# Optimization experiments

Hardware: AMD Instinct MI355X
Metric: run time of the kernel (lower is better)

The kernel has to match this reference:

```python
import jax, jax.numpy as jnp
import numpy as np

HEADS = 4
DIM_HEAD = 32
SCALE = DIM_HEAD ** -0.5

# Energy conventions (Hopfield / Lagrangian formulation):
#  Neuron(x): g = activation(x); e = sum(x*g) - L(x)
#  Synapse(g, x): e = -sum(g*x)
#  identity Lagrangian: L(x) = 0.5*sum(x^2), g = x  => Conv2d block energy = -0.5*sum(x^2)
#  softmax Lagrangian: L(x) = sum(logsumexp(x, -1)), g = softmax(x, -1)

def setup_inputs() -> dict:
    key = jax.random.key(0)
    ks = jax.random.split(key, 5)
    b, c, h, w = 8, 256, 48, 48
    hidden = HEADS * DIM_HEAD  # 128
    return {
        "x": jax.random.normal(ks[0], (b, c, h, w), jnp.float32),
        "w_qkv": jax.random.normal(ks[1], (hidden * 3, c), jnp.float32) * 0.02,
        "b_qkv": jax.random.normal(ks[2], (hidden * 3,), jnp.float32) * 0.02,
        "w_out": jax.random.normal(ks[3], (c, hidden), jnp.float32) * 0.02,
        "b_out": jax.random.normal(ks[4], (c,), jnp.float32) * 0.02,
    }

def reference(x, w_qkv, b_qkv, w_out, b_out):
    b, c, h, w = x.shape
    # 1x1 conv == channel matmul
    qkv = jnp.einsum('oc,bcxy->boxy', w_qkv, x) + b_qkv[None, :, None, None]
    e_qkv = -0.5 * jnp.sum(qkv * qkv)  # identity-Lagrangian neuron + synapse energy
    q, k, v = jnp.split(qkv, 3, axis=1)
    # 'b (h c) x y -> b h c (x y)'
    def heads(t):
        return t.reshape(b, HEADS, DIM_HEAD, h * w)
    q, k, v = heads(q), heads(k), heads(v)
    q = q * SCALE
    sim = jnp.einsum('bhdi,bhdj->bhij', q, k)  # [b, heads, hw, hw]
    sim = sim - jax.lax.stop_gradient(jnp.max(sim, axis=-1, keepdims=True))
    attn = jax.nn.softmax(sim, axis=-1)
    # softmax-Lagrangian neuron energy: sum(sim*attn) - sum(logsumexp(sim, -1))
    e_attn = jnp.sum(sim * attn) - jnp.sum(jax.nn.logsumexp(sim, axis=-1))
    out = jnp.einsum('bhij,bhdj->bhid', attn, v)  # [b, heads, hw, dim_head]
    # 'b h (x y) d -> b (h d) x y'
    out = out.transpose(0, 1, 3, 2).reshape(b, HEADS * DIM_HEAD, h, w)
    out = jnp.einsum('oc,bcxy->boxy', w_out, out) + b_out[None, :, None, None]
    e_out = -0.5 * jnp.sum(out * out)
    return out, e_attn + e_out + e_qkv
```

## Files before the change

kernel.cpp:

```cpp
#include <hip/hip_runtime.h>
#include <hip/hip_bf16.h>

#define HW 2304
#define NB 8
#define NC 256
#define HID 128
#define DH 32
#define NH 4
#define SCALE 0.17677669529663687f
#define LOG2E 1.4426950408889634f
#define LN2   0.6931471805599453f

using bf16x8 = __attribute__((ext_vector_type(8))) short;
using f32x4  = __attribute__((ext_vector_type(4))) float;

__device__ __forceinline__ short f2bf(float f) {
    unsigned u = __float_as_uint(f);
    u += 0x7FFF + ((u >> 16) & 1);
    return (short)(u >> 16);
}
__device__ __forceinline__ unsigned pk2bf(float a, float b) {
    union { __hip_bfloat162 h; unsigned u; } cv;
    cv.h = __float22bfloat162_rn(float2{a, b});
    return cv.u;
}
__device__ __forceinline__ void gld16(const void* g, void* l) {
    __builtin_amdgcn_global_load_lds(
        (const __attribute__((address_space(1))) unsigned*)g,
        (__attribute__((address_space(3))) unsigned*)l, 16, 0, 0);
}

__global__ __launch_bounds__(256)
void prep(const float* __restrict__ x, const float* __restrict__ wq,
          const float* __restrict__ wo, short* __restrict__ Xt,
          short* __restrict__ Wq, short* __restrict__ Wo, float* __restrict__ wsz)
{
    if (blockIdx.z == 8) {
        const int bid = blockIdx.x + 72 * blockIdx.y;
        if (bid == 0 && threadIdx.x == 0) { wsz[0] = 0.f; ((int*)wsz)[1] = 0; }
        const int i = bid * 256 + threadIdx.x;
        if (i < 384 * 256) Wq[i] = f2bf(wq[i]);
        if (i < 256 * 128) Wo[i] = f2bf(wo[i]);
        return;
    }
    __shared__ float T[32][33];
    const int b = blockIdx.z, c0 = blockIdx.y * 32, s0 = blockIdx.x * 32;
    const int ts = threadIdx.x & 31, tc = threadIdx.x >> 5;
    #pragma unroll
    for (int cc = tc; cc < 32; cc += 8)
        T[cc][ts] = x[((size_t)b * NC + c0 + cc) * HW + s0 + ts];
    __syncthreads();
    const int tcc = threadIdx.x & 31, tss = threadIdx.x >> 5;
    #pragma unroll
    for (int ss = tss; ss < 32; ss += 8)
        Xt[((size_t)b * HW + s0 + ss) * NC + c0 + tcc] = f2bf(T[tcc][ss]);
}

template<int KD, bool QKV>
__global__ __launch_bounds__(256, 4)
void conv_mfma(const short* __restrict__ A, const short* __restrict__ Bt,
               const float* __restrict__ bias, float* __restrict__ out0,
               short* __restrict__ Qb, short* __restrict__ Kb,
               short* __restrict__ Vb, float* __restrict__ E,
               int* __restrict__ ticket, int nblocks, float* __restrict__ edst)
{
    const int b  = blockIdx.z;
    const int bm = blockIdx.y * 64;
    const int bn = blockIdx.x * 128;
    const int t  = threadIdx.x;
    const int w  = t >> 6, lane = t & 63;
    const int n16 = lane & 15, quad = lane >> 4;

    __shared__ __align__(16) char csm[24576];
    __shared__ float red[4];

    const int rL = lane >> 2, cswz = (lane & 3) ^ (rL & 3);
    const char* agl = (const char*)(A  + (size_t)(bm + rL) * KD + cswz * 8);
    const char* bgl = (const char*)(Bt + ((size_t)b * HW + bn + rL) * KD + cswz * 8);

    auto issue = [&](int kc, int pbuf) {
        char* base = csm + pbuf * 12288;
        if (w == 0) {
            gld16(agl + (size_t)(0 * 16 * KD + kc) * 2, base + 0 * 1024);
            gld16(agl + (size_t)(1 * 16 * KD + kc) * 2, base + 1 * 1024);
            gld16(bgl + (size_t)(0 * 16 * KD + kc) * 2, base + 4096 + 0 * 1024);
        } else if (w == 1) {
            gld16(agl + (size_t)(2 * 16 * KD + kc) * 2, base + 2 * 1024);
            gld16(agl + (size_t)(3 * 16 * KD + kc) * 2, base + 3 * 1024);
            gld16(bgl + (size_t)(1 * 16 * KD + kc) * 2, base + 4096 + 1 * 1024);
        } else if (w == 2) {
            gld16(bgl + (size_t)(2 * 16 * KD + kc) * 2, base + 4096 + 2 * 1024);
            gld16(bgl + (size_t)(3 * 16 * KD + kc) * 2, base + 4096 + 3 * 1024);
            gld16(bgl + (size_t)(4 * 16 * KD + kc) * 2, base + 4096 + 4 * 1024);
        } else {
            gld16(bgl + (size_t)(5 * 16 * KD + kc) * 2, base + 4096 + 5 * 1024);
            gld16(bgl + (size_t)(6 * 16 * KD + kc) * 2, base + 4096 + 6 * 1024);
            gld16(bgl + (size_t)(7 * 16 * KD + kc) * 2, base + 4096 + 7 * 1024);
        }
    };

    f32x4 acc[4][2] = {};
    const int rsw = (quad ^ (n16 & 3)) * 16;
    constexpr int NI = KD / 32;

    issue(0, 0);
    for (int ki = 0; ki < NI; ++ki) {
        const int p = ki & 1;
        __syncthreads();
        if (ki + 1 < NI) issue((ki + 1) * 32, p ^ 1);

        const char* Ap = csm + p * 12288;
        const char* Bp = Ap + 4096;
        bf16x8 am[4], bq[2];
        #pragma unroll
        for (int tm = 0; tm < 4; ++tm)
            am[tm] = *(const bf16x8*)(Ap + tm * 1024 + n16 * 64 + rsw);
        #pragma unroll
        for (int j = 0; j < 2; ++j)
            bq[j] = *(const bf16x8*)(Bp + (w * 2 + j) * 1024 + n16 * 64 + rsw);
        #pragma unroll
        for (int tm = 0; tm < 4; ++tm)
            #pragma unroll
            for (int j = 0; j < 2; ++j)
                acc[tm][j] = __builtin_amdgcn_mfma_f32_16x16x32_bf16(am[tm], bq[j], acc[tm][j], 0, 0, 0);
    }

    float e = 0.f;
    #pragma unroll
    for (int tm = 0; tm < 4; ++tm) {
        const int o0 = bm + tm * 16 + quad * 4;
        const float4 bb = *(const float4*)(bias + o0);
        #pragma unroll
        for (int j = 0; j < 2; ++j) {
            const int s = bn + (w * 2 + j) * 16 + n16;
            float v[4] = {acc[tm][j][0] + bb.x, acc[tm][j][1] + bb.y,
                          acc[tm][j][2] + bb.z, acc[tm][j][3] + bb.w};
            e -= 0.5f * (v[0]*v[0] + v[1]*v[1] + v[2]*v[2] + v[3]*v[3]);
            if (QKV) {
                if (o0 < HID) {
                    const int h = o0 >> 5, dh0 = o0 & 31;
                    const float qs = SCALE * LOG2E;
                    short4 pk = {f2bf(v[0]*qs), f2bf(v[1]*qs),
                                 f2bf(v[2]*qs), f2bf(v[3]*qs)};
                    *(short4*)(Qb + ((size_t)(b * NH + h) * HW + s) * DH + dh0) = pk;
                } else if (o0 < 2 * HID) {
                    const int c = o0 - HID, h = c >> 5, dh0 = c & 31;
                    const int g = s & 31;
                    const int sp = (s & ~31) | ((g & 1) << 4) | (g >> 1);
                    short4 pk = {f2bf(v[0]), f2bf(v[1]), f2bf(v[2]), f2bf(v[3])};
                    *(short4*)(Kb + ((size_t)(b * NH + h) * HW + sp) * DH + dh0) = pk;
                } else {
                    const int c = o0 - 2 * HID, h = c >> 5, dh0 = c & 31;
                    #pragma unroll
                    for (int r = 0; r < 4; ++r)
                        Vb[((size_t)(b * NH + h) * DH + dh0 + r) * HW + s] = f2bf(v[r]);
                }
            } else {
                #pragma unroll
                for (int r = 0; r < 4; ++r)
                    out0[((size_t)b * NC + o0 + r) * HW + s] = v[r];
            }
        }
    }

    #pragma unroll
    for (int off = 32; off > 0; off >>= 1) e += __shfl_down(e, off);
    if (lane == 0) red[w] = e;
    __syncthreads();
    if (t == 0) {
        atomicAdd(E, red[0] + red[1] + red[2] + red[3]);
        if (!QKV) {
            __threadfence();
            const int prev = atomicAdd(ticket, 1);
            if (prev == nblocks - 1) {
                __threadfence();
                edst[0] = atomicAdd(E, 0.f);
            }
        }
    }
}

__global__ __launch_bounds__(256)
void flash7(const short* __restrict__ Qb, const short* __restrict__ Kb,
            const short* __restrict__ Vb, short* __restrict__ attT,
            float* __restrict__ E)
{
    __shared__ __align__(16) char smem[16384 + 4 * 5120];

    const int bh   = blockIdx.y;
    const int w    = threadIdx.x >> 6;
    const int lane = threadIdx.x & 63;
    const int n16  = lane & 15, quad = lane >> 4;
    const int qb   = blockIdx.x * 128 + w * 32;

    bf16x8 aq[2];
    #pragma unroll
    for (int qg = 0; qg < 2; ++qg)
        aq[qg] = *(const bf16x8*)(Qb + ((size_t)bh * HW + qb + qg * 16 + n16) * DH + quad * 8);

    const int rL = lane >> 2, cL = (lane & 3) ^ (rL & 3);
    const char* gbase; size_t gstep;
    if (w < 2) {
        gbase = (const char*)(Kb + (size_t)bh * HW * DH) + ((w & 1) * 16 + rL) * 64 + cL * 16;
        gstep = 2048;
    } else {
        gbase = (const char*)(Vb + (size_t)bh * DH * HW)
              + (size_t)((w & 1) * 16 + rL) * (HW * 2) + cL * 16;
        gstep = 64;
    }

    gld16(gbase,         smem + 0    + w * 1024);
    gld16(gbase + gstep, smem + 4096 + w * 1024);

    f32x4 acc[2][2] = {};
    float ls[2][4] = {}, ts[2][4] = {};
    const int swz = (quad ^ (n16 & 3)) * 8;
    short* Pbase = (short*)(smem + 16384) + w * 2560;

    for (int it = 0; it < 36; ++it) {
        const int p = it & 1;
        __syncthreads();
        if (it + 1 < 36) {
            const size_t g0 = (size_t)(2 * it + 2) * gstep;
            gld16(gbase + g0,         smem + (p ^ 1) * 8192 + 0    + w * 1024);
            gld16(gbase + g0 + gstep, smem + (p ^ 1) * 8192 + 4096 + w * 1024);
        }

        #pragma unroll
        for (int ca = 0; ca < 2; ++ca) {
            const short* kb = (const short*)(smem + p * 8192 + ca * 4096);
            short* Ps = Pbase + ca * 1280;
            unsigned* P32 = (unsigned*)Ps;

            const bf16x8 bk0 = *(const bf16x8*)(kb + n16 * 32 + swz);
            const bf16x8 bk1 = *(const bf16x8*)(kb + 512  + n16 * 32 + swz);
            const bf16x8 bv0 = *(const bf16x8*)(kb + 1024 + n16 * 32 + swz);
            const bf16x8 bv1 = *(const bf16x8*)(kb + 1536 + n16 * 32 + swz);

            #pragma unroll
            for (int qg = 0; qg < 2; ++qg) {
                f32x4 z = {};
                const f32x4 s0 = __builtin_amdgcn_mfma_f32_16x16x32_bf16(aq[qg], bk0, z, 0, 0, 0);
                const f32x4 s1 = __builtin_amdgcn_mfma_f32_16x16x32_bf16(aq[qg], bk1, z, 0, 0, 0);
                #pragma unroll
                for (int r = 0; r < 4; ++r) {
                    const float p0 = __builtin_amdgcn_exp2f(s0[r]);
                    const float p1 = __builtin_amdgcn_exp2f(s1[r]);
                    ls[qg][r] += p0 + p1;
                    ts[qg][r] += p0 * s0[r] + p1 * s1[r];
                    P32[(qg * 16 + quad * 4 + r) * 20 + n16] = pk2bf(p0, p1);
                }
            }
            #pragma unroll
            for (int qg = 0; qg < 2; ++qg) {
                const bf16x8 pa = *(const bf16x8*)(Ps + (qg * 16 + n16) * 40 + quad * 8);
                acc[qg][0] = __builtin_amdgcn_mfma_f32_16x16x32_bf16(pa, bv0, acc[qg][0], 0, 0, 0);
                acc[qg][1] = __builtin_amdgcn_mfma_f32_16x16x32_bf16(pa, bv1, acc[qg][1], 0, 0, 0);
            }
        }
    }

    #pragma unroll
    for (int m = 1; m < 16; m <<= 1)
        #pragma unroll
        for (int qg = 0; qg < 2; ++qg)
            #pragma unroll
            for (int r = 0; r < 4; ++r) {
                ls[qg][r] += __shfl_xor(ls[qg][r], m);
                ts[qg][r] += __shfl_xor(ts[qg][r], m);
            }

    const int bb = bh >> 2, h = bh & 3;
    float e = 0.f;
    #pragma unroll
    for (int qg = 0; qg < 2; ++qg)
        #pragma unroll
        for (int r = 0; r < 4; ++r) {
            const int q = qb + qg * 16 + quad * 4 + r;
            const float L = ls[qg][r];
            const float invl = 1.f / L;
            short* ap = attT + ((size_t)bb * HW + q) * HID + h * 32;
            ap[n16]      = f2bf(acc[qg][0][r] * invl);
            ap[n16 + 16] = f2bf(acc[qg][1][r] * invl);
            e += (LN2 * ts[qg][r]) * invl - __logf(L);
        }
    e = (n16 == 0) ? e : 0.f;
    e += __shfl_xor(e, 16);
    e += __shfl_xor(e, 32);
    if (lane == 0) atomicAdd(E, e);
}

extern "C" void kernel_launch(void* const* d_in, const int* in_sizes, int n_in,
                              void* d_out, int out_size, void* d_ws, size_t ws_size,
                              hipStream_t stream) {
    const float* x     = (const float*)d_in[0];
    const float* w_qkv = (const float*)d_in[1];
    const float* b_qkv = (const float*)d_in[2];
    const float* w_out = (const float*)d_in[3];
    const float* b_out = (const float*)d_in[4];
    float* out = (float*)d_out;

    float* wsf    = (float*)d_ws;
    float* E      = wsf;
    int*   ticket = (int*)d_ws + 1;
    short* Xt   = (short*)(wsf + 16);
    short* Wq   = Xt + (size_t)NB * HW * NC;
    short* Wo   = Wq + 384 * 256;
    short* Qb   = Wo + 256 * 128;
    short* Kb   = Qb + (size_t)NB * NH * HW * DH;
    short* Vb   = Kb + (size_t)NB * NH * HW * DH;
    short* attT = Vb + (size_t)NB * NH * HW * DH;

    prep<<<dim3(HW / 32, NC / 32, NB + 1), 256, 0, stream>>>(
        x, w_qkv, w_out, Xt, Wq, Wo, wsf);
    conv_mfma<NC, true><<<dim3(18, 6, NB), 256, 0, stream>>>(
        Wq, Xt, b_qkv, nullptr, Qb, Kb, Vb, E, nullptr, 0, nullptr);
    flash7<<<dim3(HW / 128, NB * NH), 256, 0, stream>>>(
        Qb, Kb, Vb, attT, E);
    conv_mfma<HID, false><<<dim3(18, 4, NB), 256, 0, stream>>>(
        Wo, attT, b_out, out, nullptr, nullptr, nullptr, E,
        ticket, 18 * 4 * NB, out + (size_t)NB * NC * HW);
}
```

Measured before the change: 209.7 us.

## Keep softmax probabilities in registers by transposing the QK MFMA and permuting K

The QK^T MFMA now takes K as the A operand and Q as B, so each lane holds scores for a single query row. K rows are stored with a new permutation so the exp'd values can be packed straight into the B operand of the PV MFMA. This drops the LDS round-trip for P, its shared buffer, and most of the per-row shuffle reductions. The output write and energy reduction are adjusted to the transposed accumulator layout. Correctness now depends on the K permutation exactly matching the MFMA register layout.

```diff
diff --git a/kernel.cpp b/kernel.cpp
--- a/kernel.cpp
+++ b/kernel.cpp
@@ -146,7 +146,7 @@
                 } else if (o0 < 2 * HID) {
                     const int c = o0 - HID, h = c >> 5, dh0 = c & 31;
                     const int g = s & 31;
-                    const int sp = (s & ~31) | ((g & 1) << 4) | (g >> 1);
+                    const int sp = (s & ~31) | ((g & 4) << 2) | ((g >> 3) << 2) | (g & 3);
                     short4 pk = {f2bf(v[0]), f2bf(v[1]), f2bf(v[2]), f2bf(v[3])};
                     *(short4*)(Kb + ((size_t)(b * NH + h) * HW + sp) * DH + dh0) = pk;
                 } else {
@@ -181,11 +181,11 @@
 }
 
 __global__ __launch_bounds__(256)
-void flash7(const short* __restrict__ Qb, const short* __restrict__ Kb,
+void flash9(const short* __restrict__ Qb, const short* __restrict__ Kb,
             const short* __restrict__ Vb, short* __restrict__ attT,
             float* __restrict__ E)
 {
-    __shared__ __align__(16) char smem[16384 + 4 * 5120];
+    __shared__ __align__(16) char smem[16384];
 
     const int bh   = blockIdx.y;
     const int w    = threadIdx.x >> 6;
@@ -213,9 +213,8 @@
     gld16(gbase + gstep, smem + 4096 + w * 1024);
 
     f32x4 acc[2][2] = {};
-    float ls[2][4] = {}, ts[2][4] = {};
+    float ls[2] = {}, ts[2] = {};
     const int swz = (quad ^ (n16 & 3)) * 8;
-    short* Pbase = (short*)(smem + 16384) + w * 2560;
 
     for (int it = 0; it < 36; ++it) {
         const int p = it & 1;
@@ -229,8 +228,6 @@
         #pragma unroll
         for (int ca = 0; ca < 2; ++ca) {
             const short* kb = (const short*)(smem + p * 8192 + ca * 4096);
-            short* Ps = Pbase + ca * 1280;
-            unsigned* P32 = (unsigned*)Ps;
 
             const bf16x8 bk0 = *(const bf16x8*)(kb + n16 * 32 + swz);
             const bf16x8 bk1 = *(const bf16x8*)(kb + 512  + n16 * 32 + swz);
@@ -240,53 +237,55 @@
             #pragma unroll
             for (int qg = 0; qg < 2; ++qg) {
                 f32x4 z = {};
-                const f32x4 s0 = __builtin_amdgcn_mfma_f32_16x16x32_bf16(aq[qg], bk0, z, 0, 0, 0);
-                const f32x4 s1 = __builtin_amdgcn_mfma_f32_16x16x32_bf16(aq[qg], bk1, z, 0, 0, 0);
+                const f32x4 s0 = __builtin_amdgcn_mfma_f32_16x16x32_bf16(bk0, aq[qg], z, 0, 0, 0);
+                const f32x4 s1 = __builtin_amdgcn_mfma_f32_16x16x32_bf16(bk1, aq[qg], z, 0, 0, 0);
+                float e0[4], e1[4];
                 #pragma unroll
                 for (int r = 0; r < 4; ++r) {
-                    const float p0 = __builtin_amdgcn_exp2f(s0[r]);
-                    const float p1 = __builtin_amdgcn_exp2f(s1[r]);
-                    ls[qg][r] += p0 + p1;
-                    ts[qg][r] += p0 * s0[r] + p1 * s1[r];
-                    P32[(qg * 16 + quad * 4 + r) * 20 + n16] = pk2bf(p0, p1);
+                    e0[r] = __builtin_amdgcn_exp2f(s0[r]);
+                    e1[r] = __builtin_amdgcn_exp2f(s1[r]);
                 }
+                ls[qg] += (e0[0] + e0[1]) + (e0[2] + e0[3])
+                        + (e1[0] + e1[1]) + (e1[2] + e1[3]);
+                ts[qg] += (e0[0]*s0[0] + e0[1]*s0[1]) + (e0[2]*s0[2] + e0[3]*s0[3])
+                        + (e1[0]*s1[0] + e1[1]*s1[1]) + (e1[2]*s1[2] + e1[3]*s1[3]);
+                union { bf16x8 v; unsigned u[4]; } pa;
+                pa.u[0] = pk2bf(e0[0], e0[1]);
+                pa.u[1] = pk2bf(e0[2], e0[3]);
+                pa.u[2] = pk2bf(e1[0], e1[1]);
+                pa.u[3] = pk2bf(e1[2], e1[3]);
+                acc[qg][0] = __builtin_amdgcn_mfma_f32_16x16x32_bf16(bv0, pa.v, acc[qg][0], 0, 0, 0);
+                acc[qg][1] = __builtin_amdgcn_mfma_f32_16x16x32_bf16(bv1, pa.v, acc[qg][1], 0, 0, 0);
             }
-            #pragma unroll
-            for (int qg = 0; qg < 2; ++qg) {
-                const bf16x8 pa = *(const bf16x8*)(Ps + (qg * 16 + n16) * 40 + quad * 8);
-                acc[qg][0] = __builtin_amdgcn_mfma_f32_16x16x32_bf16(pa, bv0, acc[qg][0], 0, 0, 0);
-                acc[qg][1] = __builtin_amdgcn_mfma_f32_16x16x32_bf16(pa, bv1, acc[qg][1], 0, 0, 0);
-            }
-        }
-    }
-
-    #pragma unroll
-    for (int m = 1; m < 16; m <<= 1)
-        #pragma unroll
-        for (int qg = 0; qg < 2; ++qg)
-            #pragma unroll
-            for (int r = 0; r < 4; ++r) {
-                ls[qg][r] += __shfl_xor(ls[qg][r], m);
-                ts[qg][r] += __shfl_xor(ts[qg][r], m);
-            }
+        }
+    }
+
+    #pragma unroll
+    for (int qg = 0; qg < 2; ++qg) {
+        ls[qg] += __shfl_xor(ls[qg], 16);
+        ls[qg] += __shfl_xor(ls[qg], 32);
+        ts[qg] += __shfl_xor(ts[qg], 16);
+        ts[qg] += __shfl_xor(ts[qg], 32);
+    }
 
     const int bb = bh >> 2, h = bh & 3;
     float e = 0.f;
     #pragma unroll
-    for (int qg = 0; qg < 2; ++qg)
-        #pragma unroll
-        for (int r = 0; r < 4; ++r) {
-            const int q = qb + qg * 16 + quad * 4 + r;
-            const float L = ls[qg][r];
-            const float invl = 1.f / L;
-            short* ap = attT + ((size_t)bb * HW + q) * HID + h * 32;
-            ap[n16]      = f2bf(acc[qg][0][r] * invl);
-            ap[n16 + 16] = f2bf(acc[qg][1][r] * invl);
-            e += (LN2 * ts[qg][r]) * invl - __logf(L);
-        }
-    e = (n16 == 0) ? e : 0.f;
-    e += __shfl_xor(e, 16);
-    e += __shfl_xor(e, 32);
+    for (int qg = 0; qg < 2; ++qg) {
+        const int q = qb + qg * 16 + n16;
+        const float L = ls[qg];
+        const float invl = 1.f / L;
+        short* ap = attT + ((size_t)bb * HW + q) * HID + h * 32;
+        short4 pk0 = {f2bf(acc[qg][0][0] * invl), f2bf(acc[qg][0][1] * invl),
+                      f2bf(acc[qg][0][2] * invl), f2bf(acc[qg][0][3] * invl)};
+        short4 pk1 = {f2bf(acc[qg][1][0] * invl), f2bf(acc[qg][1][1] * invl),
+                      f2bf(acc[qg][1][2] * invl), f2bf(acc[qg][1][3] * invl)};
+        *(short4*)(ap + quad * 4)      = pk0;
+        *(short4*)(ap + 16 + quad * 4) = pk1;
+        if (quad == 0) e += (LN2 * ts[qg]) * invl - __logf(L);
+    }
+    #pragma unroll
+    for (int m = 1; m < 64; m <<= 1) e += __shfl_xor(e, m);
     if (lane == 0) atomicAdd(E, e);
 }
 
@@ -315,7 +314,7 @@
         x, w_qkv, w_out, Xt, Wq, Wo, wsf);
     conv_mfma<NC, true><<<dim3(18, 6, NB), 256, 0, stream>>>(
         Wq, Xt, b_qkv, nullptr, Qb, Kb, Vb, E, nullptr, 0, nullptr);
-    flash7<<<dim3(HW / 128, NB * NH), 256, 0, stream>>>(
+    flash9<<<dim3(HW / 128, NB * NH), 256, 0, stream>>>(
         Qb, Kb, Vb, attT, E);
     conv_mfma<HID, false><<<dim3(18, 4, NB), 256, 0, stream>>>(
         Wo, attT, b_out, out, nullptr, nullptr, nullptr, E,
```

Measured after the change: 208.1 us. Within noise of the previous version (-0.8%).
